# Optimization experiments

Measured on AMD Instinct MI355X. Metric: run time of the kernel, lower is better.

The kernel has to match this reference:

```python
import jax, jax.numpy as jnp
import numpy as np
from jax import lax

K = 3  # dynamic/static conv kernel size
C = 64  # n_feat (hard-coded by Linear(64, ...) in the module)


def leaky(x):
    return jax.nn.leaky_relu(x, 0.1)


def conv2d(x, w, b, pad):
    # x: [B,C,H,W], w: [O,I,kh,kw] (OIHW), b: [O]
    y = lax.conv_general_dilated(x, w, (1, 1), [(pad, pad), (pad, pad)],
                                 dimension_numbers=("NCHW", "OIHW", "NCHW"))
    return y + b.reshape(1, -1, 1, 1)


def rda_conv(x, d, k1, k2, cw, cb):
    # x: [B,C,H,W], d: [B,64]
    b, c, h, w = x.shape
    hid = leaky(d @ k1)                        # [B,64]
    kern = (hid @ k2).reshape(b * c, 1, K, K)  # per-(batch,channel) kernel
    pad = (K - 1) // 2
    # depthwise dynamic conv: groups = b*c
    out = lax.conv_general_dilated(x.reshape(1, b * c, h, w), kern, (1, 1),
                                   [(pad, pad), (pad, pad)],
                                   feature_group_count=b * c,
                                   dimension_numbers=("NCHW", "OIHW", "NCHW"))
    out = leaky(out).reshape(b, c, h, w)
    M = jax.nn.sigmoid(conv2d(x, cw, cb, 0))   # [B,1,H,W] gating map
    return out * M + x


def setup_inputs() -> dict:
    key = jax.random.key(0)
    ks = jax.random.split(key, 14)
    s = 0.05
    inp = {
        "x": jax.random.normal(ks[0], (16, C, 128, 128), jnp.float32),
        "d": jax.random.normal(ks[1], (16, C), jnp.float32),
        # RDA_conv 1: kernel MLP (stored as [in,out]) + 1x1 gating conv
        "da1_k1": jax.random.normal(ks[2], (64, 64), jnp.float32) * s,
        "da1_k2": jax.random.normal(ks[3], (64, 64 * K * K), jnp.float32) * s,
        "da1_cw": jax.random.normal(ks[4], (1, C, 1, 1), jnp.float32) * s,
        "da1_cb": jax.random.normal(ks[5], (1,), jnp.float32) * s,
        # RDA_conv 2
        "da2_k1": jax.random.normal(ks[6], (64, 64), jnp.float32) * s,
        "da2_k2": jax.random.normal(ks[7], (64, 64 * K * K), jnp.float32) * s,
        "da2_cw": jax.random.normal(ks[8], (1, C, 1, 1), jnp.float32) * s,
        "da2_cb": jax.random.normal(ks[9], (1,), jnp.float32) * s,
        # static 3x3 convs
        "conv1_w": jax.random.normal(ks[10], (C, C, K, K), jnp.float32) * s,
        "conv1_b": jax.random.normal(ks[11], (C,), jnp.float32) * s,
        "conv2_w": jax.random.normal(ks[12], (C, C, K, K), jnp.float32) * s,
        "conv2_b": jax.random.normal(ks[13], (C,), jnp.float32) * s,
    }
    return inp


def reference(x, d, da1_k1, da1_k2, da1_cw, da1_cb, da2_k1, da2_k2, da2_cw,
              da2_cb, conv1_w, conv1_b, conv2_w, conv2_b):
    pad = (K - 1) // 2
    out = leaky(rda_conv(x, d, da1_k1, da1_k2, da1_cw, da1_cb))
    out = leaky(conv2d(out, conv1_w, conv1_b, pad))
    out = leaky(rda_conv(out, d, da2_k1, da2_k2, da2_cw, da2_cb))
    out = conv2d(out, conv2_w, conv2_b, pad) + x
    return out
```

## Files before the change

### kernel.cpp

```cpp
#include <hip/hip_runtime.h>
#include <hip/hip_bf16.h>
#include <math.h>

#define B_ 16
#define C_ 64
#define H_ 128
#define W_ 128
#define HW_ (H_*W_)
#define CHW_ (C_*HW_)
#define NTOT_ (B_*CHW_)

typedef __attribute__((ext_vector_type(8))) short short8;
typedef __attribute__((ext_vector_type(4))) float float4v;

__device__ __forceinline__ float leaky(float v) { return v > 0.f ? v : 0.1f * v; }
__device__ __forceinline__ float bs2f(short u) {
    return __uint_as_float(((unsigned)(unsigned short)u) << 16);
}
__device__ __forceinline__ short f2bs(float v) {
    __hip_bfloat16 h = __float2bfloat16(v);
    union { __hip_bfloat16 h; short s; } u; u.h = h; return u.s;
}

__global__ __launch_bounds__(256) void k_setup(
    const float* __restrict__ X, const float* __restrict__ cw,
    const float* __restrict__ cb, __hip_bfloat16* __restrict__ Xn,
    float* __restrict__ G1,
    const float* __restrict__ d,
    const float* __restrict__ k1a, const float* __restrict__ k2a,
    const float* __restrict__ k1b, const float* __restrict__ k2b,
    float* __restrict__ kernA, float* __restrict__ kernB,
    const float* __restrict__ W1, const float* __restrict__ W2,
    __hip_bfloat16* __restrict__ P1, __hip_bfloat16* __restrict__ P2)
{
    __shared__ float sT[64][65];
    __shared__ float pG[4][64];
    __shared__ float hid[64];
    const int bid = blockIdx.x;
    const int tid = threadIdx.x;

    if (bid < 4096) {
        const int b = bid >> 8;
        const int p0 = (bid & 255) * 64;
        #pragma unroll
        for (int i = 0; i < 16; ++i) {
            int idx = i*256 + tid;
            int c = idx >> 6, p = idx & 63;
            sT[c][p] = X[(size_t)b*CHW_ + (size_t)c*HW_ + p0 + p];
        }
        __syncthreads();
        #pragma unroll
        for (int i = 0; i < 16; ++i) {
            int idx = i*256 + tid;
            int p = idx >> 6, c = idx & 63;
            Xn[((size_t)b*HW_ + p0 + p)*64 + c] = __float2bfloat16(sT[c][p]);
        }
        const int cg = tid >> 6, p = tid & 63;
        float part = 0.f;
        #pragma unroll
        for (int c = 0; c < 16; ++c) part = fmaf(sT[cg*16 + c][p], cw[cg*16 + c], part);
        pG[cg][p] = part;
        __syncthreads();
        if (tid < 64) {
            float g = pG[0][tid] + pG[1][tid] + pG[2][tid] + pG[3][tid] + cb[0];
            G1[(size_t)b*HW_ + p0 + tid] = 1.f / (1.f + __expf(-g));
        }
    } else if (bid < 4192) {
        const int r2 = bid - 4096;
        const int which = r2 / 48;
        const int rr    = r2 % 48;
        const int b     = rr / 3;
        const int chunk = rr % 3;
        const float* k1 = which ? k1b : k1a;
        const float* k2 = which ? k2b : k2a;
        float* outp = which ? kernB : kernA;
        if (tid < 64) {
            float s = 0.f;
            #pragma unroll
            for (int i = 0; i < 64; ++i) s = fmaf(d[b*64 + i], k1[i*64 + tid], s);
            hid[tid] = leaky(s);
        }
        __syncthreads();
        if (tid < 192) {
            const int o = chunk * 192 + tid;
            float s = 0.f;
            #pragma unroll
            for (int j = 0; j < 64; ++j) s = fmaf(hid[j], k2[j*576 + o], s);
            outp[b*576 + (o % 9)*64 + (o / 9)] = s;
        }
    } else {
        const int p = bid - 4192;
        const int s = p % 18;
        const int which = p / 18;
        const float* W = which ? W2 : W1;
        __hip_bfloat16* P = which ? P2 : P1;
        const int t = s >> 1, hf = s & 1;
        for (int idx = tid; idx < 2048; idx += 256) {
            const int oc = idx >> 5, kk = idx & 31;
            P[s*2048 + idx] = __float2bfloat16(W[oc*576 + (hf*32 + kk)*9 + t]);
        }
    }
}

template<int MODE>
__global__ __launch_bounds__(256) void k_rda_conv(
    const __hip_bfloat16* __restrict__ Xn, const float* __restrict__ kernN,
    const float* __restrict__ G, const __hip_bfloat16* __restrict__ Wpk,
    const float* __restrict__ bias, const float* __restrict__ Xres,
    const float* __restrict__ Gcw, const float* __restrict__ Gcb,
    __hip_bfloat16* __restrict__ OutN, float* __restrict__ OutF,
    float* __restrict__ G2)
{
    __shared__ __align__(16) short sA[12*20*64];
    const int tid = threadIdx.x;
    const int b = blockIdx.y;
    const int h0 = (blockIdx.x >> 3) * 8;
    const int w0 = (blockIdx.x & 7) * 16;
    const int lane = tid & 63;
    const int wv = tid >> 6;

    const short* Xs = (const short*)Xn;
    for (int idx = tid; idx < 1920; idx += 256) {
        const int cc = idx & 7;
        const int w = (idx >> 3) % 20;
        const int r = idx / 160;
        const int gh = h0 - 2 + r;
        const int gw = w0 - 2 + w;
        uint4 v = make_uint4(0, 0, 0, 0);
        if ((unsigned)gh < (unsigned)H_ && (unsigned)gw < (unsigned)W_)
            v = *(const uint4*)(Xs + (((size_t)b*H_ + gh)*W_ + gw)*64 + cc*8);
        *(uint4*)(sA + ((r*20 + w)*64 + ((cc ^ (w & 7)) * 8))) = v;
    }

    float k9[9];
    #pragma unroll
    for (int t = 0; t < 9; ++t) k9[t] = kernN[((size_t)b*9 + t)*64 + lane];

    int loff[8];
    #pragma unroll
    for (int jc = 0; jc < 8; ++jc)
        loff[jc] = (((lane >> 3) ^ jc) << 3) + (lane & 7);

    auto compute_row = [&](int r, float* outv) {
        const int gh = h0 - 1 + r;
        if ((unsigned)gh < (unsigned)H_) {
            float gv[18];
            const float* Gp = G + (size_t)b*HW_ + (size_t)gh*W_ + (w0 - 1);
            #pragma unroll
            for (int w = 0; w < 18; ++w) {
                const int gw = w0 - 1 + w;
                gv[w] = ((unsigned)gw < (unsigned)W_) ? Gp[w] : 0.f;
            }
            #pragma unroll
            for (int w = 0; w < 18; ++w) outv[w] = 0.f;
            const short* r0 = sA + (r*20)*64;
            const short* r1 = r0 + 20*64;
            const short* r2 = r1 + 20*64;
            float c1p = 0.f;
            #pragma unroll
            for (int j = 0; j < 20; ++j) {
                const int off = j*64 + loff[j & 7];
                const float c0 = bs2f(r0[off]);
                const float c1 = bs2f(r1[off]);
                const float c2 = bs2f(r2[off]);
                #pragma unroll
                for (int dw = 0; dw < 3; ++dw) {
                    const int w = j - dw;
                    if (w >= 0 && w < 18)
                        outv[w] = fmaf(c0, k9[dw],
                                  fmaf(c1, k9[3+dw],
                                  fmaf(c2, k9[6+dw], outv[w])));
                }
                const int wf = j - 2;
                if (wf >= 0) {
                    const int gw = w0 - 1 + wf;
                    float val = 0.f;
                    if ((unsigned)gw < (unsigned)W_)
                        val = leaky(leaky(outv[wf]) * gv[wf] + c1p);
                    outv[wf] = val;
                }
                c1p = c1;
            }
        } else {
            #pragma unroll
            for (int w = 0; w < 18; ++w) outv[w] = 0.f;
        }
    };
    auto write_rowf = [&](int r, const float* ov) {
        short* wp = sA + (r*20)*64;
        #pragma unroll
        for (int w = 0; w < 18; ++w)
            wp[w*64 + loff[w & 7]] = f2bs(ov[w]);
    };

    __syncthreads();

    float outv[18];
    compute_row(wv, outv);
    __syncthreads();
    write_rowf(wv, outv);
    compute_row(4 + wv, outv);
    __syncthreads();
    write_rowf(4 + wv, outv);
    if (wv < 2) compute_row(8 + wv, outv);
    __syncthreads();
    if (wv < 2) write_rowf(8 + wv, outv);
    __syncthreads();

    const int l15 = lane & 15;
    const int lq = lane >> 4;

    float4v acc[2][4];
    #pragma unroll
    for (int i = 0; i < 2; ++i)
        #pragma unroll
        for (int j = 0; j < 4; ++j) acc[i][j] = (float4v)0.f;

    const short* Wp = (const short*)Wpk;

    #pragma unroll
    for (int s = 0; s < 18; ++s) {
        const int t = s >> 1, hf = s & 1;
        const int dh = t / 3, dwx = t % 3;
        short8 afr[2], bfr[4];
        #pragma unroll
        for (int mt = 0; mt < 2; ++mt) {
            const int r = wv*2 + mt + dh;
            const int w = l15 + dwx;
            const int chunk = (hf*4 + lq) ^ (w & 7);
            afr[mt] = *(const short8*)(sA + ((r*20 + w)*64 + chunk*8));
        }
        #pragma unroll
        for (int nt = 0; nt < 4; ++nt)
            bfr[nt] = *(const short8*)(Wp + ((size_t)s*2048 + (nt*16 + l15)*32 + lq*8));
        #pragma unroll
        for (int mt = 0; mt < 2; ++mt)
            #pragma unroll
            for (int nt = 0; nt < 4; ++nt)
                acc[mt][nt] = __builtin_amdgcn_mfma_f32_16x16x32_bf16(
                    afr[mt], bfr[nt], acc[mt][nt], 0, 0, 0);
    }

    float bs[4], cwv[4], cbv = 0.f;
    #pragma unroll
    for (int nt = 0; nt < 4; ++nt) bs[nt] = bias[nt*16 + l15];
    if (MODE == 0) {
        #pragma unroll
        for (int nt = 0; nt < 4; ++nt) cwv[nt] = Gcw[nt*16 + l15];
        cbv = Gcb[0];
    }

    #pragma unroll
    for (int mt = 0; mt < 2; ++mt) {
        const int pr = wv*2 + mt;
        if (MODE == 0) {
            float vv[4][4];
            #pragma unroll
            for (int nt = 0; nt < 4; ++nt)
                #pragma unroll
                for (int rg = 0; rg < 4; ++rg)
                    vv[nt][rg] = leaky(acc[mt][nt][rg] + bs[nt]);
            #pragma unroll
            for (int nt = 0; nt < 4; ++nt) {
                const int n = nt*16 + l15;
                #pragma unroll
                for (int rg = 0; rg < 4; ++rg) {
                    const int pw = lq*4 + rg;
                    OutN[(((size_t)b*H_ + h0 + pr)*W_ + w0 + pw)*64 + n] =
                        __float2bfloat16(vv[nt][rg]);
                }
            }
            #pragma unroll
            for (int rg = 0; rg < 4; ++rg) {
                float p = vv[0][rg]*cwv[0] + vv[1][rg]*cwv[1]
                        + vv[2][rg]*cwv[2] + vv[3][rg]*cwv[3];
                p += __shfl_xor(p, 1);
                p += __shfl_xor(p, 2);
                p += __shfl_xor(p, 4);
                p += __shfl_xor(p, 8);
                if (l15 == 0)
                    G2[(size_t)b*HW_ + (size_t)(h0 + pr)*W_ + w0 + lq*4 + rg] =
                        1.f / (1.f + __expf(-(p + cbv)));
            }
        } else {
            #pragma unroll
            for (int nt = 0; nt < 4; ++nt) {
                const int n = nt*16 + l15;
                const size_t base = ((size_t)(b*64 + n)*H_ + h0 + pr)*W_ + w0 + lq*4;
                const float4 xr = *(const float4*)(Xres + base);
                float4 v;
                v.x = acc[mt][nt][0] + bs[nt] + xr.x;
                v.y = acc[mt][nt][1] + bs[nt] + xr.y;
                v.z = acc[mt][nt][2] + bs[nt] + xr.z;
                v.w = acc[mt][nt][3] + bs[nt] + xr.w;
                *(float4*)(OutF + base) = v;
            }
        }
    }
}

extern "C" void kernel_launch(void* const* d_in, const int* in_sizes, int n_in,
                              void* d_out, int out_size, void* d_ws, size_t ws_size,
                              hipStream_t stream)
{
    const float* x       = (const float*)d_in[0];
    const float* d       = (const float*)d_in[1];
    const float* da1_k1  = (const float*)d_in[2];
    const float* da1_k2  = (const float*)d_in[3];
    const float* da1_cw  = (const float*)d_in[4];
    const float* da1_cb  = (const float*)d_in[5];
    const float* da2_k1  = (const float*)d_in[6];
    const float* da2_k2  = (const float*)d_in[7];
    const float* da2_cw  = (const float*)d_in[8];
    const float* da2_cb  = (const float*)d_in[9];
    const float* conv1_w = (const float*)d_in[10];
    const float* conv1_b = (const float*)d_in[11];
    const float* conv2_w = (const float*)d_in[12];
    const float* conv2_b = (const float*)d_in[13];
    float* out = (float*)d_out;

    __hip_bfloat16* bufA = (__hip_bfloat16*)d_ws;
    __hip_bfloat16* bufB = bufA + NTOT_;
    float* kernA = (float*)(bufB + NTOT_);
    float* kernB = kernA + 16*576;
    __hip_bfloat16* wpk1 = (__hip_bfloat16*)(kernB + 16*576);
    __hip_bfloat16* wpk2 = wpk1 + 18*64*32;
    float* G1 = (float*)(wpk2 + 18*64*32);
    float* G2 = G1 + (size_t)B_*HW_;

    k_setup<<<dim3(4228), dim3(256), 0, stream>>>(
        x, da1_cw, da1_cb, bufA, G1,
        d, da1_k1, da1_k2, da2_k1, da2_k2, kernA, kernB,
        conv1_w, conv2_w, wpk1, wpk2);
    k_rda_conv<0><<<dim3(128, B_), dim3(256), 0, stream>>>(
        bufA, kernA, G1, wpk1, conv1_b, nullptr, da2_cw, da2_cb, bufB, nullptr, G2);
    k_rda_conv<1><<<dim3(128, B_), dim3(256), 0, stream>>>(
        bufB, kernB, G2, wpk2, conv2_b, x, nullptr, nullptr, nullptr, out, nullptr);
}
```

Measured before the change: 248.7 us.

## Fuse input transpose and first gating map into first RDA conv kernel

Result: slower. 264.8 us (+6.5%).

```diff
diff --git a/kernel.cpp b/kernel.cpp
--- a/kernel.cpp
+++ b/kernel.cpp
@@ -23,9 +23,6 @@
 }
 
 __global__ __launch_bounds__(256) void k_setup(
-    const float* __restrict__ X, const float* __restrict__ cw,
-    const float* __restrict__ cb, __hip_bfloat16* __restrict__ Xn,
-    float* __restrict__ G1,
     const float* __restrict__ d,
     const float* __restrict__ k1a, const float* __restrict__ k2a,
     const float* __restrict__ k1b, const float* __restrict__ k2b,
@@ -33,42 +30,13 @@
     const float* __restrict__ W1, const float* __restrict__ W2,
     __hip_bfloat16* __restrict__ P1, __hip_bfloat16* __restrict__ P2)
 {
-    __shared__ float sT[64][65];
-    __shared__ float pG[4][64];
     __shared__ float hid[64];
     const int bid = blockIdx.x;
     const int tid = threadIdx.x;
 
-    if (bid < 4096) {
-        const int b = bid >> 8;
-        const int p0 = (bid & 255) * 64;
-        #pragma unroll
-        for (int i = 0; i < 16; ++i) {
-            int idx = i*256 + tid;
-            int c = idx >> 6, p = idx & 63;
-            sT[c][p] = X[(size_t)b*CHW_ + (size_t)c*HW_ + p0 + p];
-        }
-        __syncthreads();
-        #pragma unroll
-        for (int i = 0; i < 16; ++i) {
-            int idx = i*256 + tid;
-            int p = idx >> 6, c = idx & 63;
-            Xn[((size_t)b*HW_ + p0 + p)*64 + c] = __float2bfloat16(sT[c][p]);
-        }
-        const int cg = tid >> 6, p = tid & 63;
-        float part = 0.f;
-        #pragma unroll
-        for (int c = 0; c < 16; ++c) part = fmaf(sT[cg*16 + c][p], cw[cg*16 + c], part);
-        pG[cg][p] = part;
-        __syncthreads();
-        if (tid < 64) {
-            float g = pG[0][tid] + pG[1][tid] + pG[2][tid] + pG[3][tid] + cb[0];
-            G1[(size_t)b*HW_ + p0 + tid] = 1.f / (1.f + __expf(-g));
-        }
-    } else if (bid < 4192) {
-        const int r2 = bid - 4096;
-        const int which = r2 / 48;
-        const int rr    = r2 % 48;
+    if (bid < 96) {
+        const int which = bid / 48;
+        const int rr    = bid % 48;
         const int b     = rr / 3;
         const int chunk = rr % 3;
         const float* k1 = which ? k1b : k1a;
@@ -89,7 +57,7 @@
             outp[b*576 + (o % 9)*64 + (o / 9)] = s;
         }
     } else {
-        const int p = bid - 4192;
+        const int p = bid - 96;
         const int s = p % 18;
         const int which = p / 18;
         const float* W = which ? W2 : W1;
@@ -109,9 +77,13 @@
     const float* __restrict__ bias, const float* __restrict__ Xres,
     const float* __restrict__ Gcw, const float* __restrict__ Gcb,
     __hip_bfloat16* __restrict__ OutN, float* __restrict__ OutF,
-    float* __restrict__ G2)
+    float* __restrict__ G2,
+    const float* __restrict__ Xf, const float* __restrict__ Gcw1,
+    const float* __restrict__ Gcb1)
 {
     __shared__ __align__(16) short sA[12*20*64];
+    __shared__ float gS[10][18];
+    __shared__ float sCW[64];
     const int tid = threadIdx.x;
     const int b = blockIdx.y;
     const int h0 = (blockIdx.x >> 3) * 8;
@@ -119,17 +91,43 @@
     const int lane = tid & 63;
     const int wv = tid >> 6;
 
-    const short* Xs = (const short*)Xn;
-    for (int idx = tid; idx < 1920; idx += 256) {
-        const int cc = idx & 7;
-        const int w = (idx >> 3) % 20;
-        const int r = idx / 160;
-        const int gh = h0 - 2 + r;
-        const int gw = w0 - 2 + w;
-        uint4 v = make_uint4(0, 0, 0, 0);
-        if ((unsigned)gh < (unsigned)H_ && (unsigned)gw < (unsigned)W_)
-            v = *(const uint4*)(Xs + (((size_t)b*H_ + gh)*W_ + gw)*64 + cc*8);
-        *(uint4*)(sA + ((r*20 + w)*64 + ((cc ^ (w & 7)) * 8))) = v;
+    if (MODE == 0) {
+        if (tid < 16) *(float4*)&sCW[tid*4] = *(const float4*)&Gcw1[tid*4];
+        const float* Xb = Xf + (size_t)b*CHW_;
+        for (int idx = tid; idx < 3840; idx += 256) {
+            const int k  = idx % 10;
+            const int rc = idx / 10;
+            const int cp = rc & 31;
+            const int r  = rc >> 5;
+            const int c0 = cp*2;
+            const int gh = h0 - 2 + r;
+            const int gw = w0 - 2 + k*2;
+            float2 va = make_float2(0.f, 0.f), vb = make_float2(0.f, 0.f);
+            if ((unsigned)gh < (unsigned)H_ && (unsigned)gw < (unsigned)W_) {
+                const float* p = Xb + ((size_t)c0*H_ + gh)*W_ + gw;
+                va = *(const float2*)p;
+                vb = *(const float2*)(p + HW_);
+            }
+            const int wA = k*2, wB = k*2 + 1;
+            short2 sa, sb;
+            sa.x = f2bs(va.x); sa.y = f2bs(vb.x);
+            sb.x = f2bs(va.y); sb.y = f2bs(vb.y);
+            *(short2*)(sA + ((r*20 + wA)*64 + (((c0>>3) ^ (wA&7))*8) + (c0&7))) = sa;
+            *(short2*)(sA + ((r*20 + wB)*64 + (((c0>>3) ^ (wB&7))*8) + (c0&7))) = sb;
+        }
+    } else {
+        const short* Xs = (const short*)Xn;
+        for (int idx = tid; idx < 1920; idx += 256) {
+            const int cc = idx & 7;
+            const int w = (idx >> 3) % 20;
+            const int r = idx / 160;
+            const int gh = h0 - 2 + r;
+            const int gw = w0 - 2 + w;
+            uint4 v = make_uint4(0, 0, 0, 0);
+            if ((unsigned)gh < (unsigned)H_ && (unsigned)gw < (unsigned)W_)
+                v = *(const uint4*)(Xs + (((size_t)b*H_ + gh)*W_ + gw)*64 + cc*8);
+            *(uint4*)(sA + ((r*20 + w)*64 + ((cc ^ (w & 7)) * 8))) = v;
+        }
     }
 
     float k9[9];
@@ -140,16 +138,41 @@
     #pragma unroll
     for (int jc = 0; jc < 8; ++jc)
         loff[jc] = (((lane >> 3) ^ jc) << 3) + (lane & 7);
+
+    __syncthreads();
+
+    if (MODE == 0) {
+        if (tid < 180) {
+            const int r = tid / 18, wf = tid % 18;
+            const int sw = wf + 1;
+            const short* px = sA + (((r + 1)*20 + sw)*64);
+            float g = 0.f;
+            #pragma unroll
+            for (int cc = 0; cc < 8; ++cc) {
+                short8 v = *(const short8*)(px + ((cc ^ (sw & 7))*8));
+                #pragma unroll
+                for (int e = 0; e < 8; ++e)
+                    g = fmaf(bs2f(v[e]), sCW[cc*8 + e], g);
+            }
+            gS[r][wf] = 1.f / (1.f + __expf(-(g + Gcb1[0])));
+        }
+        __syncthreads();
+    }
 
     auto compute_row = [&](int r, float* outv) {
         const int gh = h0 - 1 + r;
         if ((unsigned)gh < (unsigned)H_) {
             float gv[18];
-            const float* Gp = G + (size_t)b*HW_ + (size_t)gh*W_ + (w0 - 1);
-            #pragma unroll
-            for (int w = 0; w < 18; ++w) {
-                const int gw = w0 - 1 + w;
-                gv[w] = ((unsigned)gw < (unsigned)W_) ? Gp[w] : 0.f;
+            if (MODE == 0) {
+                #pragma unroll
+                for (int w = 0; w < 18; ++w) gv[w] = gS[r][w];
+            } else {
+                const float* Gp = G + (size_t)b*HW_ + (size_t)gh*W_ + (w0 - 1);
+                #pragma unroll
+                for (int w = 0; w < 18; ++w) {
+                    const int gw = w0 - 1 + w;
+                    gv[w] = ((unsigned)gw < (unsigned)W_) ? Gp[w] : 0.f;
+                }
             }
             #pragma unroll
             for (int w = 0; w < 18; ++w) outv[w] = 0.f;
@@ -192,8 +215,6 @@
         for (int w = 0; w < 18; ++w)
             wp[w*64 + loff[w & 7]] = f2bs(ov[w]);
     };
-
-    __syncthreads();
 
     float outv[18];
     compute_row(wv, outv);
@@ -328,12 +349,13 @@
     float* G1 = (float*)(wpk2 + 18*64*32);
     float* G2 = G1 + (size_t)B_*HW_;
 
-    k_setup<<<dim3(4228), dim3(256), 0, stream>>>(
-        x, da1_cw, da1_cb, bufA, G1,
+    k_setup<<<dim3(132), dim3(256), 0, stream>>>(
         d, da1_k1, da1_k2, da2_k1, da2_k2, kernA, kernB,
         conv1_w, conv2_w, wpk1, wpk2);
     k_rda_conv<0><<<dim3(128, B_), dim3(256), 0, stream>>>(
-        bufA, kernA, G1, wpk1, conv1_b, nullptr, da2_cw, da2_cb, bufB, nullptr, G2);
+        nullptr, kernA, nullptr, wpk1, conv1_b, nullptr, da2_cw, da2_cb,
+        bufB, nullptr, G2, x, da1_cw, da1_cb);
     k_rda_conv<1><<<dim3(128, B_), dim3(256), 0, stream>>>(
-        bufB, kernB, G2, wpk2, conv2_b, x, nullptr, nullptr, nullptr, out, nullptr);
-}
+        bufB, kernB, G2, wpk2, conv2_b, x, nullptr, nullptr, nullptr, out,
+        nullptr, nullptr, nullptr, nullptr);
+}
```
